# Optimization experiments

Measured on AMD Instinct MI355X. Metric: run time of the kernel, lower is better.

Reference implementation:

```python
import jax, jax.numpy as jnp
import numpy as np

L, B, T, H = 3, 128, 256, 512  # layers, batch, seq_max_len, n_hidden


def setup_inputs() -> dict:
    key = jax.random.key(0)
    k0, k1, k2 = jax.random.split(key, 3)
    scale = 1.0 / np.sqrt(H).astype(np.float32)
    x = jax.random.normal(k0, (B, T, H), jnp.float32)
    kernels = jax.random.normal(k1, (L, H, 3 * H), jnp.float32) * scale
    rec_kernels = jax.random.normal(k2, (L, H, 3 * H), jnp.float32) * scale
    biases = jnp.zeros((L, 2, 3 * H), jnp.float32)  # [input_bias, recurrent_bias] (reset_after=True)
    return {"x": x, "kernels": kernels, "rec_kernels": rec_kernels, "biases": biases}


def _gru_layer(x, h0, Wk, Wu, b):
    # x: [B,T,D], h0: [B,H], Wk: [D,3H], Wu: [H,3H], b: [2,3H]
    # Keras GRU, reset_after=True, gate order (z, r, h)
    xp = jnp.einsum('btd,dh->bth', x, Wk) + b[0]  # precompute input projections
    br = b[1]

    def step(h, xp_t):
        rec = h @ Wu + br                      # [B,3H]
        xz, xr, xh = jnp.split(xp_t, 3, axis=-1)
        rz, rr, rh = jnp.split(rec, 3, axis=-1)
        z = jax.nn.sigmoid(xz + rz)
        r = jax.nn.sigmoid(xr + rr)
        hh = jnp.tanh(xh + r * rh)
        h_new = z * h + (1.0 - z) * hh
        return h_new, h_new

    last_h, seq = jax.lax.scan(step, h0, jnp.swapaxes(xp, 0, 1))  # seq: [T,B,H]
    return jnp.swapaxes(seq, 0, 1), last_h


def reference(x, kernels, rec_kernels, biases):
    Bc, Tc, _ = x.shape
    Hd = kernels.shape[2] // 3
    state = None
    for l in range(kernels.shape[0]):
        # layer l>0 receives previous layer's final state as initial_state
        h0 = jnp.zeros((Bc, Hd), x.dtype) if state is None else state
        x, state = _gru_layer(x, h0, kernels[l], rec_kernels[l], biases[l])
    # tf.reshape(states, (-1, H)) then tf.split(seq_max_len, axis=0) -> stack == reshape to [T, B, H]
    states_h = x.reshape(-1, Hd).reshape(Tc, -1, Hd)
    return states_h, state
```

## Files before the change

kernel.cpp:

```cpp
#include <hip/hip_runtime.h>
#include <hip/hip_bf16.h>

#define NL  3
#define NB  128
#define NT  256
#define NH  512
#define NH3 1536
#define NBH (NB*NH)
#define NM  (NB*NT)

typedef __bf16 bf16x8 __attribute__((ext_vector_type(8)));
typedef float  floatx4 __attribute__((ext_vector_type(4)));
typedef __hip_bfloat16 bf16;
typedef unsigned long long u64;

__device__ __forceinline__ floatx4 mfma16(bf16x8 a, bf16x8 b, floatx4 c) {
  return __builtin_amdgcn_mfma_f32_16x16x32_bf16(a, b, c, 0, 0, 0);
}
__device__ __forceinline__ void gload16(const void* g, void* l) {
  __builtin_amdgcn_global_load_lds(
      (const __attribute__((address_space(1))) unsigned int*)g,
      (__attribute__((address_space(3))) unsigned int*)l, 16, 0, 0);
}
__device__ __forceinline__ float fsig(float x)  { return 1.0f / (1.0f + __expf(-x)); }
__device__ __forceinline__ float ftanh(float x) { return 2.0f / (1.0f + __expf(-2.0f*x)) - 1.0f; }
__device__ __forceinline__ float b2f(unsigned short u) {
  unsigned v = (unsigned)u << 16; float f; __builtin_memcpy(&f, &v, 4); return f;
}
__device__ __forceinline__ unsigned short f2b(float f) {
  bf16 h = __float2bfloat16(f); unsigned short u; __builtin_memcpy(&u, &h, 2); return u;
}
__device__ __forceinline__ u64 ald(const u64* p) {
  return __hip_atomic_load(p, __ATOMIC_RELAXED, __HIP_MEMORY_SCOPE_AGENT);
}
__device__ __forceinline__ void ast(u64* p, u64 v) {
  __hip_atomic_store(p, v, __ATOMIC_RELAXED, __HIP_MEMORY_SCOPE_AGENT);
}

__global__ void transpose_cvt_kernel(const float* __restrict__ in, bf16* __restrict__ out) {
  __shared__ float tile[32][33];
  int l = blockIdx.z;
  int n0 = blockIdx.x * 32, k0 = blockIdx.y * 32;
  const float* src = in + (size_t)l * NH * NH3;
  bf16* dst = out + (size_t)l * NH3 * NH;
  int tx = threadIdx.x, ty = threadIdx.y;
#pragma unroll
  for (int i = 0; i < 4; i++)
    tile[ty + 8*i][tx] = src[(size_t)(k0 + ty + 8*i) * NH3 + n0 + tx];
  __syncthreads();
#pragma unroll
  for (int i = 0; i < 4; i++)
    dst[(size_t)(n0 + ty + 8*i) * NH + k0 + tx] = __float2bfloat16(tile[tx][ty + 8*i]);
}

__global__ void cvt_x_kernel(const float* __restrict__ in, bf16* __restrict__ out) {
  size_t i = (size_t)blockIdx.x * blockDim.x + threadIdx.x;
  float4 v = ((const float4*)in)[i];
  ushort4 pk;
  pk.x = f2b(v.x); pk.y = f2b(v.y); pk.z = f2b(v.z); pk.w = f2b(v.w);
  ((ushort4*)out)[i] = pk;
}

__global__ void __launch_bounds__(256, 2) gemm_xp_kernel(
    const bf16* __restrict__ A, const bf16* __restrict__ Bt,
    const float* __restrict__ bias, bf16* __restrict__ C, int a_mode)
{
  __shared__ char alds[16384];
  __shared__ char blds[16384];
  int tid = threadIdx.x;
  int lane = tid & 63, w = tid >> 6;
  int mblk = blockIdx.x, nblk = blockIdx.y;
  int wm = w >> 1, wn = w & 1;
  int klane = (lane >> 4) * 8;
  int r0 = 2*w*16 + (lane & 15);
  size_t arow0, arow1;
  if (a_mode == 0) {
    arow0 = ((size_t)r0 * NT + mblk) * NH;
    arow1 = ((size_t)(r0 + 16) * NT + mblk) * NH;
  } else {
    arow0 = (size_t)(mblk*128 + r0) * NH;
    arow1 = arow0 + (size_t)16 * NH;
  }
  size_t brow0 = (size_t)(nblk*128 + 2*w*16 + (lane & 15)) * NH;
  size_t brow1 = brow0 + (size_t)16 * NH;

  floatx4 acc[4][4];
#pragma unroll
  for (int i = 0; i < 4; i++)
#pragma unroll
    for (int j = 0; j < 4; j++) acc[i][j] = (floatx4){0.f, 0.f, 0.f, 0.f};

  for (int kk = 0; kk < 8; kk++) {
    int kb = kk*64 + klane;
#pragma unroll
    for (int kt = 0; kt < 2; kt++) {
      int kg = kb + kt*32;
      gload16(A  + arow0 + kg, alds + (kt*8 + 2*w    ) * 1024);
      gload16(A  + arow1 + kg, alds + (kt*8 + 2*w + 1) * 1024);
      gload16(Bt + brow0 + kg, blds + (kt*8 + 2*w    ) * 1024);
      gload16(Bt + brow1 + kg, blds + (kt*8 + 2*w + 1) * 1024);
    }
    __syncthreads();
#pragma unroll
    for (int kt = 0; kt < 2; kt++) {
      bf16x8 af[4], bfr[4];
#pragma unroll
      for (int i = 0; i < 4; i++) af[i]  = *(const bf16x8*)(alds + ((kt*8 + wm*4 + i)*64 + lane)*16);
#pragma unroll
      for (int j = 0; j < 4; j++) bfr[j] = *(const bf16x8*)(blds + ((kt*8 + wn*4 + j)*64 + lane)*16);
#pragma unroll
      for (int i = 0; i < 4; i++)
#pragma unroll
        for (int j = 0; j < 4; j++)
          acc[i][j] = mfma16(af[i], bfr[j], acc[i][j]);
    }
    __syncthreads();
  }
  int cl = lane & 15, rbase = (lane >> 4) * 4;
#pragma unroll
  for (int i = 0; i < 4; i++) {
    int gm = mblk*128 + wm*64 + i*16 + rbase;
#pragma unroll
    for (int j = 0; j < 4; j++) {
      int gn = nblk*128 + wn*64 + j*16 + cl;
      float bv = bias[gn];
#pragma unroll
      for (int r = 0; r < 4; r++)
        C[(size_t)(gm + r) * NH3 + gn] = __float2bfloat16(acc[i][j][r] + bv);
    }
  }
}

__global__ void __launch_bounds__(512, 2) gru_scan_kernel(
    const bf16*  __restrict__ wuT,
    const float* __restrict__ br,
    const bf16*  __restrict__ xp,
    bf16*        __restrict__ seq,
    float*       __restrict__ hlast,
    float*       __restrict__ out,
    unsigned*    __restrict__ cnt,
    unsigned tgtbase, int layer)
{
  __shared__ __align__(16) char h_raw[16384];
  __shared__ int deadflag;
  int tid = threadIdx.x, lane = tid & 63, w = tid >> 6;
  int g = blockIdx.x >> 2, c = blockIdx.x & 3;
  int bb0 = g * 16;
  int r16 = lane & 15, h4 = lane >> 4;
  int srow = tid & 15, ssc = tid >> 4;
  if (tid == 0) deadflag = 0;

  bf16x8 wf[3][16];
  float  bv[3][4];
#pragma unroll
  for (int G = 0; G < 3; G++) {
    const bf16* wrow = wuT + ((size_t)(G*NH + c*128 + w*16 + r16)) * NH + h4*8;
#pragma unroll
    for (int kt = 0; kt < 16; kt++) wf[G][kt] = *(const bf16x8*)(wrow + kt*32);
#pragma unroll
    for (int q = 0; q < 4; q++) bv[G][q] = br[G*NH + c*128 + w*16 + h4*4 + q];
  }

  float hreg[4];
  if (layer == 0) {
    hreg[0] = hreg[1] = hreg[2] = hreg[3] = 0.0f;
  } else {
    const float* hsrc = hlast + (size_t)(bb0 + r16) * NH + c*128 + w*16 + h4*4;
    float4 v = *(const float4*)hsrc;
    hreg[0] = v.x; hreg[1] = v.y; hreg[2] = v.z; hreg[3] = v.w;
  }

  u64* seqU = (u64*)seq;

  for (int t = 0; t < NT; t++) {
    const u64* xq = (const u64*)(xp + ((size_t)t*NB + bb0 + r16)*NH3 + c*128 + w*16 + h4*4);
    u64 xv0 = xq[0], xv1 = xq[128], xv2 = xq[256];

    if (t > 0) {
      if (tid == 0) {
        unsigned tgt = tgtbase + 4u * (unsigned)t;
        long sp = 0;
        while (__hip_atomic_load(cnt + g, __ATOMIC_RELAXED, __HIP_MEMORY_SCOPE_AGENT) < tgt) {
          __builtin_amdgcn_s_sleep(1);
          if (++sp > (1L << 22)) { deadflag = 1; break; }
        }
      }
      __syncthreads();
      if (deadflag) return;
    }

    if (layer == 0 && t == 0) {
      *(int4*)(h_raw + tid*32)      = (int4){0,0,0,0};
      *(int4*)(h_raw + tid*32 + 16) = (int4){0,0,0,0};
    } else {
      int slot = (t == 0) ? NT : t;
      const u64* src = seqU + ((size_t)slot*NBH + (size_t)(bb0 + srow)*NH) / 4;
#pragma unroll
      for (int d = 0; d < 2; d++) {
        int sc = ssc + d*32;
        u64 q0 = ald(src + sc*2), q1 = ald(src + sc*2 + 1);
        u64* dst = (u64*)(h_raw + (((sc >> 2)*64) + (sc & 3)*16 + srow)*16);
        dst[0] = q0; dst[1] = q1;
      }
    }
    __syncthreads();

    floatx4 ac0 = (floatx4){0,0,0,0}, ac1 = (floatx4){0,0,0,0}, ac2 = (floatx4){0,0,0,0};
#pragma unroll
    for (int kt = 0; kt < 16; kt++) {
      bf16x8 hb = *(const bf16x8*)(h_raw + (kt*64 + lane)*16);
      ac0 = mfma16(wf[0][kt], hb, ac0);
      ac1 = mfma16(wf[1][kt], hb, ac1);
      ac2 = mfma16(wf[2][kt], hb, ac2);
    }

    unsigned short pk[4];
#pragma unroll
    for (int q = 0; q < 4; q++) {
      float rz = ac0[q] + bv[0][q];
      float rr = ac1[q] + bv[1][q];
      float rh = ac2[q] + bv[2][q];
      float xz = b2f((unsigned short)(xv0 >> (16*q)));
      float xr = b2f((unsigned short)(xv1 >> (16*q)));
      float xh = b2f((unsigned short)(xv2 >> (16*q)));
      float z  = fsig(xz + rz);
      float r  = fsig(xr + rr);
      float hh = ftanh(xh + r * rh);
      float hn = z * hreg[q] + (1.0f - z) * hh;
      hreg[q] = hn;
      pk[q] = f2b(hn);
    }
    u64 pv; __builtin_memcpy(&pv, pk, 8);
    ast(seqU + ((size_t)(t+1)*NBH + (size_t)(bb0 + r16)*NH)/4 + c*32 + w*4 + h4, pv);

    if (layer == 2) {
      float* o = out + ((size_t)(bb0 + r16)*NT + t)*NH + c*128 + w*16 + h4*4;
      *(float4*)o = (float4){hreg[0], hreg[1], hreg[2], hreg[3]};
      if (t == NT - 1) {
        float* o2 = out + (size_t)NM*NH + (size_t)(bb0 + r16)*NH + c*128 + w*16 + h4*4;
        *(float4*)o2 = (float4){hreg[0], hreg[1], hreg[2], hreg[3]};
      }
    } else if (t == NT - 1) {
      float* o = hlast + (size_t)(bb0 + r16)*NH + c*128 + w*16 + h4*4;
      *(float4*)o = (float4){hreg[0], hreg[1], hreg[2], hreg[3]};
    }

    __syncthreads();
    if (tid == 0 && t < NT - 1)
      __hip_atomic_fetch_add(cnt + g, 1u, __ATOMIC_RELAXED, __HIP_MEMORY_SCOPE_AGENT);
  }
}

extern "C" void kernel_launch(void* const* d_in, const int* in_sizes, int n_in,
                              void* d_out, int out_size, void* d_ws, size_t ws_size,
                              hipStream_t stream) {
  const float* x   = (const float*)d_in[0];
  const float* wk  = (const float*)d_in[1];
  const float* wu  = (const float*)d_in[2];
  const float* bis = (const float*)d_in[3];
  float* out = (float*)d_out;

  const size_t REQ = 144048192;
  if (ws_size < REQ) {
    hipMemsetAsync(d_out, 0, (size_t)out_size * 4, stream);
    return;
  }
  char* ws = (char*)d_ws;
  bf16*  wkT   = (bf16*)(ws);
  bf16*  wuT   = (bf16*)(ws + 4718592);
  bf16*  xp    = (bf16*)(ws + 9437184);
  bf16*  seq   = (bf16*)(ws + 110100480);
  bf16*  xb    = seq;
  float* hlast = (float*)(ws + 143785984);
  unsigned* cnt = (unsigned*)(ws + 144048128);

  hipMemsetAsync(cnt, 0, 64, stream);
  transpose_cvt_kernel<<<dim3(48,16,3), dim3(32,8), 0, stream>>>(wk, wkT);
  transpose_cvt_kernel<<<dim3(48,16,3), dim3(32,8), 0, stream>>>(wu, wuT);
  cvt_x_kernel<<<(NM*NH/4)/256, 256, 0, stream>>>(x, xb);

  const size_t WS = (size_t)NH3 * NH;

  gemm_xp_kernel<<<dim3(256,12), 256, 0, stream>>>(xb, wkT, bis + 0*2*NH3, xp, 0);
  gru_scan_kernel<<<32, 512, 0, stream>>>(wuT, bis + 0*2*NH3 + NH3, xp,
      seq, hlast, nullptr, cnt, 0u, 0);
  gemm_xp_kernel<<<dim3(256,12), 256, 0, stream>>>(seq + NBH, wkT + WS, bis + 1*2*NH3, xp, 1);
  gru_scan_kernel<<<32, 512, 0, stream>>>(wuT + WS, bis + 1*2*NH3 + NH3, xp,
      seq, hlast, nullptr, cnt, 1020u, 1);
  gemm_xp_kernel<<<dim3(256,12), 256, 0, stream>>>(seq + NBH, wkT + 2*WS, bis + 2*2*NH3, xp, 1);
  gru_scan_kernel<<<32, 512, 0, stream>>>(wuT + 2*WS, bis + 2*2*NH3 + NH3, xp,
      seq, hlast, out, cnt, 2040u, 2);

  (void)in_sizes; (void)n_in; (void)out_size; (void)ws_size;
}
```

Measured before the change: 3.499 ms.

## Replace shared counter barrier with per-block flags and keep own slice in LDS

The scan's inter-block synchronization moves from a single atomic counter polled by one thread (with sleep) to per-block monotonic flags, each on its own padded line. All waves poll the three peer flags directly without sleeping, and the block-wide barrier before the global reads is removed. Each block writes its own new hidden slice straight into a double-buffered LDS copy, so it only reloads the other three blocks' slices from global memory. This shortens the per-timestep critical path of the sequential recurrence, at the cost of more polling traffic and doubled LDS use.

```diff
diff --git a/kernel.cpp b/kernel.cpp
--- a/kernel.cpp
+++ b/kernel.cpp
@@ -34,6 +34,12 @@
   return __hip_atomic_load(p, __ATOMIC_RELAXED, __HIP_MEMORY_SCOPE_AGENT);
 }
 __device__ __forceinline__ void ast(u64* p, u64 v) {
+  __hip_atomic_store(p, v, __ATOMIC_RELAXED, __HIP_MEMORY_SCOPE_AGENT);
+}
+__device__ __forceinline__ unsigned aldc(const unsigned* p) {
+  return __hip_atomic_load(p, __ATOMIC_RELAXED, __HIP_MEMORY_SCOPE_AGENT);
+}
+__device__ __forceinline__ void astc(unsigned* p, unsigned v) {
   __hip_atomic_store(p, v, __ATOMIC_RELAXED, __HIP_MEMORY_SCOPE_AGENT);
 }
 
@@ -138,10 +144,10 @@
     bf16*        __restrict__ seq,
     float*       __restrict__ hlast,
     float*       __restrict__ out,
-    unsigned*    __restrict__ cnt,
-    unsigned tgtbase, int layer)
+    unsigned*    __restrict__ flags,
+    unsigned fbase, int layer)
 {
-  __shared__ __align__(16) char h_raw[16384];
+  __shared__ __align__(16) char h_raw[2][16384];
   __shared__ int deadflag;
   int tid = threadIdx.x, lane = tid & 63, w = tid >> 6;
   int g = blockIdx.x >> 2, c = blockIdx.x & 3;
@@ -170,45 +176,63 @@
     hreg[0] = v.x; hreg[1] = v.y; hreg[2] = v.z; hreg[3] = v.w;
   }
 
+  int sc_own = c*16 + w*2 + (h4 >> 1);
+  int own_off = (((sc_own >> 2)*64) + (sc_own & 3)*16 + r16)*16 + (h4 & 1)*8;
+
   u64* seqU = (u64*)seq;
+  const unsigned* myflags = flags + (g*4 + (lane & 3))*16;
+  unsigned* myflag = flags + (g*4 + c)*16;
 
   for (int t = 0; t < NT; t++) {
+    char* buf  = h_raw[t & 1];
+    char* bufN = h_raw[(t + 1) & 1];
+
     const u64* xq = (const u64*)(xp + ((size_t)t*NB + bb0 + r16)*NH3 + c*128 + w*16 + h4*4);
     u64 xv0 = xq[0], xv1 = xq[128], xv2 = xq[256];
 
     if (t > 0) {
-      if (tid == 0) {
-        unsigned tgt = tgtbase + 4u * (unsigned)t;
-        long sp = 0;
-        while (__hip_atomic_load(cnt + g, __ATOMIC_RELAXED, __HIP_MEMORY_SCOPE_AGENT) < tgt) {
-          __builtin_amdgcn_s_sleep(1);
-          if (++sp > (1L << 22)) { deadflag = 1; break; }
+      bool need = (lane < 4) && (lane != c);
+      unsigned tgt = fbase + (unsigned)t;
+      long sp = 0;
+      for (;;) {
+        bool ok = !need || (aldc(myflags) >= tgt);
+        if (__all(ok)) break;
+        if (++sp > (1L << 20)) { if (need) deadflag = 1; break; }
+      }
+      const u64* src = seqU + ((size_t)t*NBH + (size_t)(bb0 + srow)*NH) / 4;
+#pragma unroll
+      for (int d = 0; d < 2; d++) {
+        int sc = ssc + d*32;
+        if ((sc >> 4) != c) {
+          u64 q0 = ald(src + sc*2), q1 = ald(src + sc*2 + 1);
+          u64* dst = (u64*)(buf + (((sc >> 2)*64) + (sc & 3)*16 + srow)*16);
+          dst[0] = q0; dst[1] = q1;
         }
       }
-      __syncthreads();
-      if (deadflag) return;
-    }
-
-    if (layer == 0 && t == 0) {
-      *(int4*)(h_raw + tid*32)      = (int4){0,0,0,0};
-      *(int4*)(h_raw + tid*32 + 16) = (int4){0,0,0,0};
+    } else if (layer == 0) {
+#pragma unroll
+      for (int d = 0; d < 2; d++) {
+        int sc = ssc + d*32;
+        u64* dst = (u64*)(buf + (((sc >> 2)*64) + (sc & 3)*16 + srow)*16);
+        dst[0] = 0ull; dst[1] = 0ull;
+      }
     } else {
-      int slot = (t == 0) ? NT : t;
-      const u64* src = seqU + ((size_t)slot*NBH + (size_t)(bb0 + srow)*NH) / 4;
+      const u64* src = seqU + ((size_t)NT*NBH + (size_t)(bb0 + srow)*NH) / 4;
 #pragma unroll
       for (int d = 0; d < 2; d++) {
         int sc = ssc + d*32;
         u64 q0 = ald(src + sc*2), q1 = ald(src + sc*2 + 1);
-        u64* dst = (u64*)(h_raw + (((sc >> 2)*64) + (sc & 3)*16 + srow)*16);
+        u64* dst = (u64*)(buf + (((sc >> 2)*64) + (sc & 3)*16 + srow)*16);
         dst[0] = q0; dst[1] = q1;
       }
     }
     __syncthreads();
+    if (deadflag) return;
 
     floatx4 ac0 = (floatx4){0,0,0,0}, ac1 = (floatx4){0,0,0,0}, ac2 = (floatx4){0,0,0,0};
 #pragma unroll
     for (int kt = 0; kt < 16; kt++) {
-      bf16x8 hb = *(const bf16x8*)(h_raw + (kt*64 + lane)*16);
+      bf16x8 hb = *(const bf16x8*)(buf + (kt*64 + lane)*16);
       ac0 = mfma16(wf[0][kt], hb, ac0);
       ac1 = mfma16(wf[1][kt], hb, ac1);
       ac2 = mfma16(wf[2][kt], hb, ac2);
@@ -232,6 +256,7 @@
     }
     u64 pv; __builtin_memcpy(&pv, pk, 8);
     ast(seqU + ((size_t)(t+1)*NBH + (size_t)(bb0 + r16)*NH)/4 + c*32 + w*4 + h4, pv);
+    *(u64*)(bufN + own_off) = pv;
 
     if (layer == 2) {
       float* o = out + ((size_t)(bb0 + r16)*NT + t)*NH + c*128 + w*16 + h4*4;
@@ -247,7 +272,7 @@
 
     __syncthreads();
     if (tid == 0 && t < NT - 1)
-      __hip_atomic_fetch_add(cnt + g, 1u, __ATOMIC_RELAXED, __HIP_MEMORY_SCOPE_AGENT);
+      astc(myflag, fbase + (unsigned)(t + 1));
   }
 }
 
@@ -260,7 +285,7 @@
   const float* bis = (const float*)d_in[3];
   float* out = (float*)d_out;
 
-  const size_t REQ = 144048192;
+  const size_t REQ = 144050176;
   if (ws_size < REQ) {
     hipMemsetAsync(d_out, 0, (size_t)out_size * 4, stream);
     return;
@@ -272,9 +297,9 @@
   bf16*  seq   = (bf16*)(ws + 110100480);
   bf16*  xb    = seq;
   float* hlast = (float*)(ws + 143785984);
-  unsigned* cnt = (unsigned*)(ws + 144048128);
-
-  hipMemsetAsync(cnt, 0, 64, stream);
+  unsigned* flags = (unsigned*)(ws + 144048128);
+
+  hipMemsetAsync(flags, 0, 2048, stream);
   transpose_cvt_kernel<<<dim3(48,16,3), dim3(32,8), 0, stream>>>(wk, wkT);
   transpose_cvt_kernel<<<dim3(48,16,3), dim3(32,8), 0, stream>>>(wu, wuT);
   cvt_x_kernel<<<(NM*NH/4)/256, 256, 0, stream>>>(x, xb);
@@ -283,13 +308,13 @@
 
   gemm_xp_kernel<<<dim3(256,12), 256, 0, stream>>>(xb, wkT, bis + 0*2*NH3, xp, 0);
   gru_scan_kernel<<<32, 512, 0, stream>>>(wuT, bis + 0*2*NH3 + NH3, xp,
-      seq, hlast, nullptr, cnt, 0u, 0);
+      seq, hlast, nullptr, flags, 0u, 0);
   gemm_xp_kernel<<<dim3(256,12), 256, 0, stream>>>(seq + NBH, wkT + WS, bis + 1*2*NH3, xp, 1);
   gru_scan_kernel<<<32, 512, 0, stream>>>(wuT + WS, bis + 1*2*NH3 + NH3, xp,
-      seq, hlast, nullptr, cnt, 1020u, 1);
+      seq, hlast, nullptr, flags, 256u, 1);
   gemm_xp_kernel<<<dim3(256,12), 256, 0, stream>>>(seq + NBH, wkT + 2*WS, bis + 2*2*NH3, xp, 1);
   gru_scan_kernel<<<32, 512, 0, stream>>>(wuT + 2*WS, bis + 2*2*NH3 + NH3, xp,
-      seq, hlast, out, cnt, 2040u, 2);
+      seq, hlast, out, flags, 512u, 2);
 
   (void)in_sizes; (void)n_in; (void)out_size; (void)ws_size;
 }
```

New measurement: 3.857 ms. 1.1x slower.
